# Kernel tuning notes

Measured on AMD Instinct MI355X. Metric: run time of the kernel, lower is better.

Reference implementation:

```python
import jax, jax.numpy as jnp
import numpy as np

EMBED = 1024
HEADS = 16
HEAD_DIM = EMBED // HEADS
N, SEQ = 4, 2048


def setup_inputs() -> dict:
    key = jax.random.key(0)
    ks = jax.random.split(key, 9)
    values = jax.random.normal(ks[0], (N, SEQ, EMBED), dtype=jnp.float32)
    keys = jax.random.normal(ks[1], (N, SEQ, EMBED), dtype=jnp.float32)
    query = jax.random.normal(ks[2], (N, SEQ, EMBED), dtype=jnp.float32)
    mask = jax.random.randint(ks[3], (N, 1, SEQ, SEQ), 0, 2, dtype=jnp.int32)
    s_h = 1.0 / np.sqrt(HEAD_DIM)
    s_e = 1.0 / np.sqrt(EMBED)
    Wv = jax.random.normal(ks[4], (HEAD_DIM, HEAD_DIM), dtype=jnp.float32) * s_h
    Wk = jax.random.normal(ks[5], (HEAD_DIM, HEAD_DIM), dtype=jnp.float32) * s_h
    Wq = jax.random.normal(ks[6], (HEAD_DIM, HEAD_DIM), dtype=jnp.float32) * s_h
    Wo = jax.random.normal(ks[7], (EMBED, EMBED), dtype=jnp.float32) * s_e
    bo = jax.random.normal(ks[8], (EMBED,), dtype=jnp.float32) * 0.01
    return {"values": values, "keys": keys, "query": query, "mask": mask,
            "Wv": Wv, "Wk": Wk, "Wq": Wq, "Wo": Wo, "bo": bo}


def reference(values, keys, query, mask, Wv, Wk, Wq, Wo, bo):
    n, q_len = query.shape[0], query.shape[1]
    k_len, v_len = keys.shape[1], values.shape[1]
    # split heads: [N, L, H, D]
    v = values.reshape(n, v_len, HEADS, HEAD_DIM)
    k = keys.reshape(n, k_len, HEADS, HEAD_DIM)
    q = query.reshape(n, q_len, HEADS, HEAD_DIM)
    # per-head linear projections (nn.Linear: x @ W.T)
    v = jnp.einsum('nlhd,ed->nlhe', v, Wv)
    k = jnp.einsum('nlhd,ed->nlhe', k, Wk)
    q = jnp.einsum('nlhd,ed->nlhe', q, Wq)
    # [N, H, Q, K] scores
    energy = jnp.einsum('nqhd,nkhd->nhqk', q, k)
    energy = jnp.where(mask == 0, jnp.float32(-1e20), energy)
    # note: original scales by sqrt(embed_size), not sqrt(head_dim)
    attention = jax.nn.softmax(energy / jnp.sqrt(jnp.float32(EMBED)), axis=3)
    out = jnp.einsum('nhql,nlhd->nqhd', attention, v).reshape(n, q_len, EMBED)
    return out @ Wo.T + bo
```

## Files before the change

### kernel.cpp

```cpp
#include <hip/hip_runtime.h>
#include <hip/hip_bf16.h>

typedef __attribute__((ext_vector_type(8))) short bfx8;
typedef __attribute__((ext_vector_type(4))) float fx4;

#define MFMA16(a,b,c) __builtin_amdgcn_mfma_f32_16x16x32_bf16((a),(b),(c),0,0,0)

__device__ __forceinline__ unsigned short bfc(float x){
  return __builtin_bit_cast(unsigned short, __float2bfloat16(x));
}
__device__ __forceinline__ unsigned pack2(float a, float b){
  return (unsigned)bfc(a) | ((unsigned)bfc(b) << 16);
}

__device__ __forceinline__ bfx8 cvt8(const float* p){
  const float4* q = (const float4*)p;
  float4 a = q[0], b = q[1];
  bfx8 r;
  r[0]=(short)bfc(a.x); r[1]=(short)bfc(a.y); r[2]=(short)bfc(a.z); r[3]=(short)bfc(a.w);
  r[4]=(short)bfc(b.x); r[5]=(short)bfc(b.y); r[6]=(short)bfc(b.z); r[7]=(short)bfc(b.w);
  return r;
}

__device__ __forceinline__ void g2l16(const void* g, void* l){
  __builtin_amdgcn_global_load_lds((const __attribute__((address_space(1))) unsigned*)g,
                                   (__attribute__((address_space(3))) unsigned*)l, 16, 0, 0);
}

#define SCL 0.04508422002778f

__global__ __launch_bounds__(256) void pack_k(const int* __restrict__ M, const float* __restrict__ Wo,
                                              unsigned long long* __restrict__ mT,
                                              unsigned short* __restrict__ Wob){
  int bid = blockIdx.x, tid = threadIdx.x;
  if (bid < 1024){
    int l = tid & 63, wv = tid >> 6;
    int task = bid*4 + wv;
    int n = task >> 10, rem = task & 1023, kt = rem >> 5, qc = rem & 31;
    int qbase = qc*64;
    const int* mp = M + (size_t)n*2048*2048 + (size_t)kt*64 + l;
    unsigned long long myw = 0;
    for (int qq = 0; qq < 64; ++qq){
      unsigned long long b = __ballot(mp[(size_t)(qbase+qq)*2048] != 0);
      if (l == qq) myw = b;
    }
    mT[((size_t)n*32 + kt)*2048 + qbase + l] = myw;
  } else {
    int i = ((bid-1024)*256 + tid)*8;
    bfx8 v = cvt8(Wo + i);
    *(bfx8*)(Wob + i) = v;
  }
}

__global__ __launch_bounds__(256) void proj_k(const float* __restrict__ Xv, const float* __restrict__ Xk,
                                              const float* __restrict__ Xq,
                                              const float* __restrict__ Wv, const float* __restrict__ Wk,
                                              const float* __restrict__ Wq,
                                              unsigned short* __restrict__ Vt, unsigned short* __restrict__ Kb,
                                              unsigned short* __restrict__ Qb){
  int bid = blockIdx.x;
  int which = bid >> 10;
  int r = bid & 1023;
  int nh = r >> 4, sb = r & 15;
  int n = nh >> 4, h = nh & 15;
  int tid = threadIdx.x, l = tid & 63, wv = tid >> 6, g = l >> 4, j = l & 15;
  const float* X = (which==0) ? Xv : ((which==1) ? Xk : Xq);
  const float* W = (which==0) ? Wv : ((which==1) ? Wk : Wq);
  int s0 = sb*128 + wv*32;
  size_t xbase = (size_t)n*2048*1024 + (size_t)h*64;

  if (which){
    float sc = (which==2) ? SCL : 1.0f;
    bfx8 bw[4][2];
    for (int nt=0;nt<4;++nt) for (int ks=0;ks<2;++ks)
      bw[nt][ks] = cvt8(W + (nt*16 + j)*64 + ks*32 + g*8);
    bfx8 ax[2][2];
    for (int mt=0;mt<2;++mt){
      const float* xp = X + xbase + (size_t)(s0 + mt*16 + j)*1024;
      for (int ks=0;ks<2;++ks) ax[mt][ks] = cvt8(xp + ks*32 + g*8);
    }
    fx4 acc[2][4];
    for (int mt=0;mt<2;++mt) for (int nt=0;nt<4;++nt) acc[mt][nt] = (fx4){0.f,0.f,0.f,0.f};
    for (int mt=0;mt<2;++mt) for (int nt=0;nt<4;++nt) for (int ks=0;ks<2;++ks)
      acc[mt][nt] = MFMA16(ax[mt][ks], bw[nt][ks], acc[mt][nt]);
    unsigned short* O = ((which==1) ? Kb : Qb) + (size_t)nh*2048*64;
    for (int mt=0;mt<2;++mt) for (int nt=0;nt<4;++nt) for (int rr=0;rr<4;++rr){
      int s = s0 + mt*16 + g*4 + rr, e = nt*16 + j;
      O[(size_t)s*64 + e] = bfc(acc[mt][nt][rr]*sc);
    }
  } else {
    bfx8 aw[4][2];
    for (int mt=0;mt<4;++mt) for (int ks=0;ks<2;++ks)
      aw[mt][ks] = cvt8(W + (mt*16 + j)*64 + ks*32 + g*8);
    bfx8 bx[2][2];
    for (int nt=0;nt<2;++nt){
      const float* xp = X + xbase + (size_t)(s0 + nt*16 + j)*1024;
      for (int ks=0;ks<2;++ks) bx[nt][ks] = cvt8(xp + ks*32 + g*8);
    }
    fx4 acc[4][2];
    for (int mt=0;mt<4;++mt) for (int nt=0;nt<2;++nt) acc[mt][nt] = (fx4){0.f,0.f,0.f,0.f};
    for (int mt=0;mt<4;++mt) for (int nt=0;nt<2;++nt) for (int ks=0;ks<2;++ks)
      acc[mt][nt] = MFMA16(aw[mt][ks], bx[nt][ks], acc[mt][nt]);
    unsigned short* O = Vt + (size_t)nh*64*2048;
    for (int mt=0;mt<4;++mt) for (int nt=0;nt<2;++nt) for (int rr=0;rr<4;++rr){
      int d = mt*16 + g*4 + rr, s = s0 + nt*16 + j;
      O[(size_t)d*2048 + s] = bfc(acc[mt][nt][rr]);
    }
  }
}

__global__ __launch_bounds__(512, 4) void flash_k(const unsigned short* __restrict__ Qb,
                                                  const unsigned short* __restrict__ Kb,
                                                  const unsigned short* __restrict__ Vt,
                                                  const unsigned long long* __restrict__ mT,
                                                  unsigned short* __restrict__ AO){
  __shared__ short lK[2][64*64];
  __shared__ short lV[2][64*64];
  __shared__ unsigned lP[8][1024];
  int tid = threadIdx.x;
  int l = tid & 63, wv = tid >> 6, g = l >> 4, j = l & 15;
  int bid = blockIdx.x;
  int nh = bid >> 3, qb = bid & 7;
  int n = nh >> 4, h = nh & 15;
  const unsigned short* Qp = Qb + (size_t)nh*2048*64;
  const unsigned short* Kp = Kb + (size_t)nh*2048*64;
  const unsigned short* Vp = Vt + (size_t)nh*64*2048;
  int q0 = qb*256 + wv*32 + j;
  bfx8 qf0[2], qf1[2];
  qf0[0] = *(const bfx8*)(Qp + (size_t)q0*64 + g*8);
  qf0[1] = *(const bfx8*)(Qp + (size_t)q0*64 + 32 + g*8);
  qf1[0] = *(const bfx8*)(Qp + (size_t)(q0+16)*64 + g*8);
  qf1[1] = *(const bfx8*)(Qp + (size_t)(q0+16)*64 + 32 + g*8);
  bfx8 ones;
  #pragma unroll
  for (int i=0;i<8;++i) ones[i] = (short)0x3F80;
  fx4 accO0[4], accO1[4];
  #pragma unroll
  for (int mt=0;mt<4;++mt){ accO0[mt] = (fx4){0.f,0.f,0.f,0.f}; accO1[mt] = (fx4){0.f,0.f,0.f,0.f}; }
  fx4 acc5a = (fx4){0.f,0.f,0.f,0.f};
  fx4 acc5b = (fx4){0.f,0.f,0.f,0.f};
  const int swz = (j & 7) << 4;
  const unsigned long long* mrow0 = mT + (size_t)n*32*2048 + q0;

  int sidx = wv*64 + l;
  int srow = sidx >> 3, scs = (sidx & 7) ^ (srow & 7);
  const unsigned short* Ksrc = Kp + (size_t)srow*64 + scs*8;
  const unsigned short* Vsrc = Vp + (size_t)srow*2048 + scs*8;

  #define STAGE(b, kt) do { \
    g2l16(Ksrc + (size_t)(kt)*4096, (char*)lK[b] + sidx*16); \
    g2l16(Vsrc + (size_t)(kt)*64,   (char*)lV[b] + sidx*16); \
  } while(0)

  STAGE(0, 0);
  __syncthreads();
  int b = 0;

  for (int kt = 0; kt < 32; ++kt){
    if (kt < 31) STAGE(b^1, kt+1);
    unsigned long long mw0 = mrow0[(size_t)kt*2048];
    unsigned long long mw1 = mrow0[(size_t)kt*2048 + 16];
    fx4 st0[4], st1[4];
    #pragma unroll
    for (int mt=0;mt<4;++mt){
      fx4 z0 = (fx4){0.f,0.f,0.f,0.f}, z1 = (fx4){0.f,0.f,0.f,0.f};
      #pragma unroll
      for (int ks=0;ks<2;++ks){
        bfx8 kf = *(const bfx8*)((const char*)lK[b] + (mt*16+j)*128 + ((ks*64 + g*16) ^ swz));
        z0 = MFMA16(kf, qf0[ks], z0);
        z1 = MFMA16(kf, qf1[ks], z1);
      }
      st0[mt] = z0; st1[mt] = z1;
    }
    unsigned* Pb = lP[wv];
    #pragma unroll
    for (int mt=0;mt<4;++mt){
      unsigned mq = (unsigned)(mw0 >> (mt*16 + g*4)) & 0xFu;
      float p0 = __builtin_amdgcn_exp2f(((mq>>0)&1u) ? st0[mt][0] : -1e30f);
      float p1 = __builtin_amdgcn_exp2f(((mq>>1)&1u) ? st0[mt][1] : -1e30f);
      float p2 = __builtin_amdgcn_exp2f(((mq>>2)&1u) ? st0[mt][2] : -1e30f);
      float p3 = __builtin_amdgcn_exp2f(((mq>>3)&1u) ? st0[mt][3] : -1e30f);
      int b0 = mt*32 + g*8;
      int addr = j*128 + ((((b0 >> 4)) ^ (j & 7)) << 4) + (b0 & 15);
      uint2 w; w.x = pack2(p0, p1); w.y = pack2(p2, p3);
      *(uint2*)((char*)Pb + addr) = w;
    }
    #pragma unroll
    for (int mt=0;mt<4;++mt){
      unsigned mq = (unsigned)(mw1 >> (mt*16 + g*4)) & 0xFu;
      float p0 = __builtin_amdgcn_exp2f(((mq>>0)&1u) ? st1[mt][0] : -1e30f);
      float p1 = __builtin_amdgcn_exp2f(((mq>>1)&1u) ? st1[mt][1] : -1e30f);
      float p2 = __builtin_amdgcn_exp2f(((mq>>2)&1u) ? st1[mt][2] : -1e30f);
      float p3 = __builtin_amdgcn_exp2f(((mq>>3)&1u) ? st1[mt][3] : -1e30f);
      int b0 = mt*32 + g*8;
      int addr = 2048 + j*128 + ((((b0 >> 4)) ^ (j & 7)) << 4) + (b0 & 15);
      uint2 w; w.x = pack2(p0, p1); w.y = pack2(p2, p3);
      *(uint2*)((char*)Pb + addr) = w;
    }
    bfx8 pf0[2], pf1[2];
    #pragma unroll
    for (int k2=0;k2<2;++k2){
      int boff = k2*64 + g*16;
      int addr = j*128 + ((((boff>>4)) ^ (j&7)) << 4);
      pf0[k2] = *(const bfx8*)((const char*)Pb + addr);
      pf1[k2] = *(const bfx8*)((const char*)Pb + 2048 + addr);
    }
    #pragma unroll
    for (int mt=0;mt<4;++mt)
      #pragma unroll
      for (int k2=0;k2<2;++k2){
        bfx8 vf = *(const bfx8*)((const char*)lV[b] + (mt*16+j)*128 + ((k2*64 + g*16) ^ swz));
        accO0[mt] = MFMA16(vf, pf0[k2], accO0[mt]);
        accO1[mt] = MFMA16(vf, pf1[k2], accO1[mt]);
      }
    acc5a = MFMA16(ones, pf0[0], acc5a);
    acc5a = MFMA16(ones, pf0[1], acc5a);
    acc5b = MFMA16(ones, pf1[0], acc5b);
    acc5b = MFMA16(ones, pf1[1], acc5b);
    __syncthreads();
    b ^= 1;
  }
  #undef STAGE

  float inv0 = 1.0f / acc5a[0];
  float inv1 = 1.0f / acc5b[0];
  size_t tok0 = (size_t)n*2048 + (size_t)qb*256 + wv*32 + j;
  #pragma unroll
  for (int mt=0;mt<4;++mt){
    ushort4 o;
    o.x = bfc(accO0[mt][0]*inv0); o.y = bfc(accO0[mt][1]*inv0);
    o.z = bfc(accO0[mt][2]*inv0); o.w = bfc(accO0[mt][3]*inv0);
    *(ushort4*)(AO + tok0*1024 + h*64 + mt*16 + g*4) = o;
    ushort4 o1;
    o1.x = bfc(accO1[mt][0]*inv1); o1.y = bfc(accO1[mt][1]*inv1);
    o1.z = bfc(accO1[mt][2]*inv1); o1.w = bfc(accO1[mt][3]*inv1);
    *(ushort4*)(AO + (tok0+16)*1024 + h*64 + mt*16 + g*4) = o1;
  }
}

__global__ __launch_bounds__(256) void gemm_k(const unsigned short* __restrict__ AO,
                                              const unsigned short* __restrict__ Wob,
                                              const float* __restrict__ bo, float* __restrict__ out){
  __shared__ short lA[2][128*32], lB[2][128*32];
  int tid = threadIdx.x, l = tid & 63, wv = tid >> 6, g = l >> 4, j = l & 15;
  int wr = wv >> 1, wc = wv & 1;
  int bid = blockIdx.x;
  int m0 = (bid >> 3)*128, n0 = (bid & 7)*128;
  fx4 acc[4][4];
  #pragma unroll
  for (int mt=0;mt<4;++mt) for (int nt=0;nt<4;++nt) acc[mt][nt] = (fx4){0.f,0.f,0.f,0.f};

  int sbase = wv*128;
  int sidx0 = sbase + l, sidx1 = sbase + 64 + l;
  int srow0 = sidx0 >> 2, sc0 = sidx0 & 3;
  int srow1 = sidx1 >> 2, sc1 = sidx1 & 3;
  const unsigned short* Asrc0 = AO  + (size_t)(m0+srow0)*1024 + sc0*8;
  const unsigned short* Asrc1 = AO  + (size_t)(m0+srow1)*1024 + sc1*8;
  const unsigned short* Bsrc0 = Wob + (size_t)(n0+srow0)*1024 + sc0*8;
  const unsigned short* Bsrc1 = Wob + (size_t)(n0+srow1)*1024 + sc1*8;

  #define GSTAGE(b, kb) do { \
    g2l16(Asrc0 + (kb)*32, (char*)lA[b] + sidx0*16); \
    g2l16(Asrc1 + (kb)*32, (char*)lA[b] + sidx1*16); \
    g2l16(Bsrc0 + (kb)*32, (char*)lB[b] + sidx0*16); \
    g2l16(Bsrc1 + (kb)*32, (char*)lB[b] + sidx1*16); \
  } while(0)

  GSTAGE(0, 0);
  __syncthreads();
  int b = 0;
  for (int kb = 0; kb < 32; ++kb){
    if (kb < 31) GSTAGE(b^1, kb+1);
    bfx8 af[4], bfr[4];
    #pragma unroll
    for (int mt=0;mt<4;++mt) af[mt]  = *(const bfx8*)((const char*)lA[b] + (wr*64 + mt*16 + j)*64 + g*16);
    #pragma unroll
    for (int nt=0;nt<4;++nt) bfr[nt] = *(const bfx8*)((const char*)lB[b] + (wc*64 + nt*16 + j)*64 + g*16);
    #pragma unroll
    for (int mt=0;mt<4;++mt)
      #pragma unroll
      for (int nt=0;nt<4;++nt)
        acc[mt][nt] = MFMA16(af[mt], bfr[nt], acc[mt][nt]);
    __syncthreads();
    b ^= 1;
  }
  #undef GSTAGE

  #pragma unroll
  for (int mt=0;mt<4;++mt)
    #pragma unroll
    for (int nt=0;nt<4;++nt){
      int mm = m0 + wr*64 + mt*16 + g*4;
      int oo = n0 + wc*64 + nt*16 + j;
      float bb = bo[oo];
      #pragma unroll
      for (int rr=0;rr<4;++rr)
        out[(size_t)(mm+rr)*1024 + oo] = acc[mt][nt][rr] + bb;
    }
}

extern "C" void kernel_launch(void* const* d_in, const int* in_sizes, int n_in,
                              void* d_out, int out_size, void* d_ws, size_t ws_size,
                              hipStream_t stream){
  const float* V  = (const float*)d_in[0];
  const float* K  = (const float*)d_in[1];
  const float* Q  = (const float*)d_in[2];
  const int*   M  = (const int*)d_in[3];
  const float* Wv = (const float*)d_in[4];
  const float* Wk = (const float*)d_in[5];
  const float* Wq = (const float*)d_in[6];
  const float* Wo = (const float*)d_in[7];
  const float* bo = (const float*)d_in[8];

  char* ws = (char*)d_ws;
  unsigned short* Qb = (unsigned short*)(ws + ((size_t)0  << 20));
  unsigned short* Kb = (unsigned short*)(ws + ((size_t)16 << 20));
  unsigned short* Vt = (unsigned short*)(ws + ((size_t)32 << 20));
  unsigned short* AO = (unsigned short*)(ws + ((size_t)48 << 20));
  unsigned long long* mT = (unsigned long long*)(ws + ((size_t)64 << 20));
  unsigned short* Wob = (unsigned short*)(ws + ((size_t)66 << 20));

  hipLaunchKernelGGL(pack_k,  dim3(1536), dim3(256), 0, stream, M, Wo, mT, Wob);
  hipLaunchKernelGGL(proj_k,  dim3(3072), dim3(256), 0, stream, V, K, Q, Wv, Wk, Wq, Vt, Kb, Qb);
  hipLaunchKernelGGL(flash_k, dim3(512),  dim3(512), 0, stream, Qb, Kb, Vt, mT, AO);
  hipLaunchKernelGGL(gemm_k,  dim3(512),  dim3(256), 0, stream, AO, Wob, bo, (float*)d_out);
}
```

Baseline: 202.0 us.

## Switch flash attention to 32x32 MFMA with register P-shuffle and merge prep kernels

Rewrites the attention kernel around 32x32x16 bf16 MFMA tiles. The probability tile now goes from the score accumulator to the PV operand through a lane xor-32 shuffle in registers, which removes the per-wave LDS staging buffer. The row sum is now accumulated in scalar registers instead of through extra MFMAs with a ones vector, and the mask is applied by bitmasking the exp result. The mask-pack and projection kernels are also fused into one launch to save a kernel boundary. The risks are higher register pressure from the 16-wide accumulators and the cost of the shuffles.

```diff
diff --git a/kernel.cpp b/kernel.cpp
--- a/kernel.cpp
+++ b/kernel.cpp
@@ -3,8 +3,11 @@
 
 typedef __attribute__((ext_vector_type(8))) short bfx8;
 typedef __attribute__((ext_vector_type(4))) float fx4;
+typedef __attribute__((ext_vector_type(16))) float f32x16;
+typedef __attribute__((ext_vector_type(4))) unsigned u32x4;
 
 #define MFMA16(a,b,c) __builtin_amdgcn_mfma_f32_16x16x32_bf16((a),(b),(c),0,0,0)
+#define MFMA32(a,b,c) __builtin_amdgcn_mfma_f32_32x32x16_bf16((a),(b),(c),0,0,0)
 
 __device__ __forceinline__ unsigned short bfc(float x){
   return __builtin_bit_cast(unsigned short, __float2bfloat16(x));
@@ -12,7 +15,6 @@
 __device__ __forceinline__ unsigned pack2(float a, float b){
   return (unsigned)bfc(a) | ((unsigned)bfc(b) << 16);
 }
-
 __device__ __forceinline__ bfx8 cvt8(const float* p){
   const float4* q = (const float4*)p;
   float4 a = q[0], b = q[1];
@@ -21,49 +23,59 @@
   r[4]=(short)bfc(b.x); r[5]=(short)bfc(b.y); r[6]=(short)bfc(b.z); r[7]=(short)bfc(b.w);
   return r;
 }
-
 __device__ __forceinline__ void g2l16(const void* g, void* l){
   __builtin_amdgcn_global_load_lds((const __attribute__((address_space(1))) unsigned*)g,
                                    (__attribute__((address_space(3))) unsigned*)l, 16, 0, 0);
 }
+__device__ __forceinline__ float mexp(float zv, unsigned mws, int pos){
+  float e = __builtin_amdgcn_exp2f(zv);
+  unsigned msk = (unsigned)(((int)(mws << (31-pos))) >> 31);
+  return __builtin_bit_cast(float, __builtin_bit_cast(unsigned, e) & msk);
+}
+__device__ __forceinline__ f32x16 zero16(){
+  f32x16 z;
+  #pragma unroll
+  for (int i=0;i<16;++i) z[i] = 0.f;
+  return z;
+}
 
 #define SCL 0.04508422002778f
 
-__global__ __launch_bounds__(256) void pack_k(const int* __restrict__ M, const float* __restrict__ Wo,
-                                              unsigned long long* __restrict__ mT,
-                                              unsigned short* __restrict__ Wob){
-  int bid = blockIdx.x, tid = threadIdx.x;
-  if (bid < 1024){
-    int l = tid & 63, wv = tid >> 6;
-    int task = bid*4 + wv;
-    int n = task >> 10, rem = task & 1023, kt = rem >> 5, qc = rem & 31;
-    int qbase = qc*64;
-    const int* mp = M + (size_t)n*2048*2048 + (size_t)kt*64 + l;
-    unsigned long long myw = 0;
-    for (int qq = 0; qq < 64; ++qq){
-      unsigned long long b = __ballot(mp[(size_t)(qbase+qq)*2048] != 0);
-      if (l == qq) myw = b;
-    }
-    mT[((size_t)n*32 + kt)*2048 + qbase + l] = myw;
-  } else {
-    int i = ((bid-1024)*256 + tid)*8;
-    bfx8 v = cvt8(Wo + i);
-    *(bfx8*)(Wob + i) = v;
-  }
-}
-
-__global__ __launch_bounds__(256) void proj_k(const float* __restrict__ Xv, const float* __restrict__ Xk,
+__global__ __launch_bounds__(256) void prep_k(const float* __restrict__ Xv, const float* __restrict__ Xk,
                                               const float* __restrict__ Xq,
                                               const float* __restrict__ Wv, const float* __restrict__ Wk,
                                               const float* __restrict__ Wq,
+                                              const int* __restrict__ M, const float* __restrict__ Wo,
                                               unsigned short* __restrict__ Vt, unsigned short* __restrict__ Kb,
-                                              unsigned short* __restrict__ Qb){
+                                              unsigned short* __restrict__ Qb,
+                                              unsigned long long* __restrict__ mT,
+                                              unsigned short* __restrict__ Wob){
   int bid = blockIdx.x;
+  int tid = threadIdx.x, l = tid & 63, wv = tid >> 6, g = l >> 4, j = l & 15;
+  if (bid >= 3072){
+    int pid = bid - 3072;
+    if (pid < 1024){
+      int task = pid*4 + wv;
+      int n = task >> 10, rem = task & 1023, kt = rem >> 5, qc = rem & 31;
+      int qbase = qc*64;
+      const int* mp = M + (size_t)n*2048*2048 + (size_t)kt*64 + l;
+      unsigned long long myw = 0;
+      for (int qq = 0; qq < 64; ++qq){
+        unsigned long long b = __ballot(mp[(size_t)(qbase+qq)*2048] != 0);
+        if (l == qq) myw = b;
+      }
+      mT[((size_t)n*32 + kt)*2048 + qbase + l] = myw;
+    } else {
+      int i = ((pid-1024)*256 + tid)*8;
+      bfx8 v = cvt8(Wo + i);
+      *(bfx8*)(Wob + i) = v;
+    }
+    return;
+  }
   int which = bid >> 10;
   int r = bid & 1023;
   int nh = r >> 4, sb = r & 15;
   int n = nh >> 4, h = nh & 15;
-  int tid = threadIdx.x, l = tid & 63, wv = tid >> 6, g = l >> 4, j = l & 15;
   const float* X = (which==0) ? Xv : ((which==1) ? Xk : Xq);
   const float* W = (which==0) ? Wv : ((which==1) ? Wk : Wq);
   int s0 = sb*128 + wv*32;
@@ -116,125 +128,110 @@
                                                   unsigned short* __restrict__ AO){
   __shared__ short lK[2][64*64];
   __shared__ short lV[2][64*64];
-  __shared__ unsigned lP[8][1024];
   int tid = threadIdx.x;
-  int l = tid & 63, wv = tid >> 6, g = l >> 4, j = l & 15;
+  int l = tid & 63, wv = tid >> 6, hi = l >> 5, c = l & 31;
+  int cl7 = c & 7, hi4 = hi*4;
   int bid = blockIdx.x;
   int nh = bid >> 3, qb = bid & 7;
   int n = nh >> 4, h = nh & 15;
-  const unsigned short* Qp = Qb + (size_t)nh*2048*64;
-  const unsigned short* Kp = Kb + (size_t)nh*2048*64;
-  const unsigned short* Vp = Vt + (size_t)nh*64*2048;
-  int q0 = qb*256 + wv*32 + j;
-  bfx8 qf0[2], qf1[2];
-  qf0[0] = *(const bfx8*)(Qp + (size_t)q0*64 + g*8);
-  qf0[1] = *(const bfx8*)(Qp + (size_t)q0*64 + 32 + g*8);
-  qf1[0] = *(const bfx8*)(Qp + (size_t)(q0+16)*64 + g*8);
-  qf1[1] = *(const bfx8*)(Qp + (size_t)(q0+16)*64 + 32 + g*8);
-  bfx8 ones;
-  #pragma unroll
-  for (int i=0;i<8;++i) ones[i] = (short)0x3F80;
-  fx4 accO0[4], accO1[4];
-  #pragma unroll
-  for (int mt=0;mt<4;++mt){ accO0[mt] = (fx4){0.f,0.f,0.f,0.f}; accO1[mt] = (fx4){0.f,0.f,0.f,0.f}; }
-  fx4 acc5a = (fx4){0.f,0.f,0.f,0.f};
-  fx4 acc5b = (fx4){0.f,0.f,0.f,0.f};
-  const int swz = (j & 7) << 4;
-  const unsigned long long* mrow0 = mT + (size_t)n*32*2048 + q0;
+  const unsigned short* Qp = Qb + (size_t)nh*131072;
+  const unsigned short* Kp = Kb + (size_t)nh*131072;
+  const unsigned short* Vp = Vt + (size_t)nh*131072;
+  int q = qb*256 + wv*32 + c;
+  bfx8 qf[4];
+  #pragma unroll
+  for (int s=0;s<4;++s) qf[s] = *(const bfx8*)(Qp + (size_t)q*64 + s*16 + hi*8);
+  f32x16 accO0 = zero16(), accO1 = zero16();
+  float ls = 0.f;
+  const unsigned long long* mrow = mT + (size_t)n*65536 + q;
+  int rowK0 = c*128;
+  int rowK1 = rowK0 + 4096;
 
   int sidx = wv*64 + l;
   int srow = sidx >> 3, scs = (sidx & 7) ^ (srow & 7);
   const unsigned short* Ksrc = Kp + (size_t)srow*64 + scs*8;
   const unsigned short* Vsrc = Vp + (size_t)srow*2048 + scs*8;
 
-  #define STAGE(b, kt) do { \
-    g2l16(Ksrc + (size_t)(kt)*4096, (char*)lK[b] + sidx*16); \
-    g2l16(Vsrc + (size_t)(kt)*64,   (char*)lV[b] + sidx*16); \
+  g2l16(Ksrc, (char*)lK[0] + sidx*16);
+  g2l16(Vsrc, (char*)lV[0] + sidx*16);
+  __syncthreads();
+
+#define PROC_TILE(zz, mws, TT, VB) do { \
+    unsigned Wt[8]; \
+    _Pragma("unroll") \
+    for (int wi=0; wi<8; ++wi){ \
+      const int r0 = 2*wi; \
+      const int pos = (r0&3) + 8*(r0>>2); \
+      float p0_ = mexp((zz)[r0],   (mws), pos); \
+      float p1_ = mexp((zz)[r0+1], (mws), pos+1); \
+      ls += p0_ + p1_; \
+      Wt[wi] = pack2(p0_, p1_); \
+    } \
+    _Pragma("unroll") \
+    for (int mm=0; mm<2; ++mm){ \
+      unsigned xa = hi ? Wt[4*mm+0] : Wt[4*mm+2]; \
+      unsigned xb = hi ? Wt[4*mm+1] : Wt[4*mm+3]; \
+      unsigned ra = (unsigned)__shfl_xor((int)xa, 32); \
+      unsigned rb = (unsigned)__shfl_xor((int)xb, 32); \
+      u32x4 pw; \
+      pw.x = hi ? ra : Wt[4*mm+0]; \
+      pw.y = hi ? rb : Wt[4*mm+1]; \
+      pw.z = hi ? Wt[4*mm+2] : ra; \
+      pw.w = hi ? Wt[4*mm+3] : rb; \
+      bfx8 pb = __builtin_bit_cast(bfx8, pw); \
+      const int ch2 = 2*((TT)*2+mm); \
+      bfx8 vf0 = *(const bfx8*)((VB) + rowK0 + (((ch2+hi) ^ cl7) << 4)); \
+      bfx8 vf1 = *(const bfx8*)((VB) + rowK1 + (((ch2+hi) ^ cl7) << 4)); \
+      accO0 = MFMA32(vf0, pb, accO0); \
+      accO1 = MFMA32(vf1, pb, accO1); \
+    } \
   } while(0)
 
-  STAGE(0, 0);
-  __syncthreads();
-  int b = 0;
-
-  for (int kt = 0; kt < 32; ++kt){
-    if (kt < 31) STAGE(b^1, kt+1);
-    unsigned long long mw0 = mrow0[(size_t)kt*2048];
-    unsigned long long mw1 = mrow0[(size_t)kt*2048 + 16];
-    fx4 st0[4], st1[4];
-    #pragma unroll
-    for (int mt=0;mt<4;++mt){
-      fx4 z0 = (fx4){0.f,0.f,0.f,0.f}, z1 = (fx4){0.f,0.f,0.f,0.f};
-      #pragma unroll
-      for (int ks=0;ks<2;++ks){
-        bfx8 kf = *(const bfx8*)((const char*)lK[b] + (mt*16+j)*128 + ((ks*64 + g*16) ^ swz));
-        z0 = MFMA16(kf, qf0[ks], z0);
-        z1 = MFMA16(kf, qf1[ks], z1);
-      }
-      st0[mt] = z0; st1[mt] = z1;
-    }
-    unsigned* Pb = lP[wv];
-    #pragma unroll
-    for (int mt=0;mt<4;++mt){
-      unsigned mq = (unsigned)(mw0 >> (mt*16 + g*4)) & 0xFu;
-      float p0 = __builtin_amdgcn_exp2f(((mq>>0)&1u) ? st0[mt][0] : -1e30f);
-      float p1 = __builtin_amdgcn_exp2f(((mq>>1)&1u) ? st0[mt][1] : -1e30f);
-      float p2 = __builtin_amdgcn_exp2f(((mq>>2)&1u) ? st0[mt][2] : -1e30f);
-      float p3 = __builtin_amdgcn_exp2f(((mq>>3)&1u) ? st0[mt][3] : -1e30f);
-      int b0 = mt*32 + g*8;
-      int addr = j*128 + ((((b0 >> 4)) ^ (j & 7)) << 4) + (b0 & 15);
-      uint2 w; w.x = pack2(p0, p1); w.y = pack2(p2, p3);
-      *(uint2*)((char*)Pb + addr) = w;
-    }
-    #pragma unroll
-    for (int mt=0;mt<4;++mt){
-      unsigned mq = (unsigned)(mw1 >> (mt*16 + g*4)) & 0xFu;
-      float p0 = __builtin_amdgcn_exp2f(((mq>>0)&1u) ? st1[mt][0] : -1e30f);
-      float p1 = __builtin_amdgcn_exp2f(((mq>>1)&1u) ? st1[mt][1] : -1e30f);
-      float p2 = __builtin_amdgcn_exp2f(((mq>>2)&1u) ? st1[mt][2] : -1e30f);
-      float p3 = __builtin_amdgcn_exp2f(((mq>>3)&1u) ? st1[mt][3] : -1e30f);
-      int b0 = mt*32 + g*8;
-      int addr = 2048 + j*128 + ((((b0 >> 4)) ^ (j & 7)) << 4) + (b0 & 15);
-      uint2 w; w.x = pack2(p0, p1); w.y = pack2(p2, p3);
-      *(uint2*)((char*)Pb + addr) = w;
-    }
-    bfx8 pf0[2], pf1[2];
-    #pragma unroll
-    for (int k2=0;k2<2;++k2){
-      int boff = k2*64 + g*16;
-      int addr = j*128 + ((((boff>>4)) ^ (j&7)) << 4);
-      pf0[k2] = *(const bfx8*)((const char*)Pb + addr);
-      pf1[k2] = *(const bfx8*)((const char*)Pb + 2048 + addr);
-    }
-    #pragma unroll
-    for (int mt=0;mt<4;++mt)
-      #pragma unroll
-      for (int k2=0;k2<2;++k2){
-        bfx8 vf = *(const bfx8*)((const char*)lV[b] + (mt*16+j)*128 + ((k2*64 + g*16) ^ swz));
-        accO0[mt] = MFMA16(vf, pf0[k2], accO0[mt]);
-        accO1[mt] = MFMA16(vf, pf1[k2], accO1[mt]);
-      }
-    acc5a = MFMA16(ones, pf0[0], acc5a);
-    acc5a = MFMA16(ones, pf0[1], acc5a);
-    acc5b = MFMA16(ones, pf1[0], acc5b);
-    acc5b = MFMA16(ones, pf1[1], acc5b);
-    __syncthreads();
-    b ^= 1;
-  }
-  #undef STAGE
-
-  float inv0 = 1.0f / acc5a[0];
-  float inv1 = 1.0f / acc5b[0];
-  size_t tok0 = (size_t)n*2048 + (size_t)qb*256 + wv*32 + j;
-  #pragma unroll
-  for (int mt=0;mt<4;++mt){
+#define ATTN_ITER(BUF, NBUF, kt) do { \
+    if ((kt) < 31){ \
+      g2l16(Ksrc + (size_t)((kt)+1)*4096, (char*)lK[NBUF] + sidx*16); \
+      g2l16(Vsrc + (size_t)((kt)+1)*64,   (char*)lV[NBUF] + sidx*16); \
+    } \
+    unsigned long long mw = mrow[(size_t)(kt)*2048]; \
+    const char* KB = (const char*)lK[BUF]; \
+    const char* VB = (const char*)lV[BUF]; \
+    f32x16 z0 = zero16(), z1 = zero16(); \
+    _Pragma("unroll") \
+    for (int s=0; s<4; ++s){ \
+      bfx8 kf0 = *(const bfx8*)(KB + rowK0 + (((2*s+hi) ^ cl7) << 4)); \
+      bfx8 kf1 = *(const bfx8*)(KB + rowK1 + (((2*s+hi) ^ cl7) << 4)); \
+      z0 = MFMA32(kf0, qf[s], z0); \
+      z1 = MFMA32(kf1, qf[s], z1); \
+    } \
+    unsigned mws0 = ((unsigned)mw) >> hi4; \
+    unsigned mws1 = ((unsigned)(mw >> 32)) >> hi4; \
+    PROC_TILE(z0, mws0, 0, VB); \
+    PROC_TILE(z1, mws1, 1, VB); \
+    __syncthreads(); \
+  } while(0)
+
+  #pragma unroll 1
+  for (int kt2 = 0; kt2 < 32; kt2 += 2){
+    ATTN_ITER(0, 1, kt2);
+    ATTN_ITER(1, 0, kt2+1);
+  }
+#undef ATTN_ITER
+#undef PROC_TILE
+
+  ls += __shfl_xor(ls, 32);
+  float inv = 1.0f / ls;
+  unsigned short* aop = AO + ((size_t)n*2048 + q)*1024 + h*64;
+  #pragma unroll
+  for (int u=0; u<4; ++u){
+    int d0 = u*8 + hi4;
     ushort4 o;
-    o.x = bfc(accO0[mt][0]*inv0); o.y = bfc(accO0[mt][1]*inv0);
-    o.z = bfc(accO0[mt][2]*inv0); o.w = bfc(accO0[mt][3]*inv0);
-    *(ushort4*)(AO + tok0*1024 + h*64 + mt*16 + g*4) = o;
+    o.x = bfc(accO0[4*u+0]*inv); o.y = bfc(accO0[4*u+1]*inv);
+    o.z = bfc(accO0[4*u+2]*inv); o.w = bfc(accO0[4*u+3]*inv);
+    *(ushort4*)(aop + d0) = o;
     ushort4 o1;
-    o1.x = bfc(accO1[mt][0]*inv1); o1.y = bfc(accO1[mt][1]*inv1);
-    o1.z = bfc(accO1[mt][2]*inv1); o1.w = bfc(accO1[mt][3]*inv1);
-    *(ushort4*)(AO + (tok0+16)*1024 + h*64 + mt*16 + g*4) = o1;
+    o1.x = bfc(accO1[4*u+0]*inv); o1.y = bfc(accO1[4*u+1]*inv);
+    o1.z = bfc(accO1[4*u+2]*inv); o1.w = bfc(accO1[4*u+3]*inv);
+    *(ushort4*)(aop + 32 + d0) = o1;
   }
 }
 
@@ -320,8 +317,8 @@
   unsigned long long* mT = (unsigned long long*)(ws + ((size_t)64 << 20));
   unsigned short* Wob = (unsigned short*)(ws + ((size_t)66 << 20));
 
-  hipLaunchKernelGGL(pack_k,  dim3(1536), dim3(256), 0, stream, M, Wo, mT, Wob);
-  hipLaunchKernelGGL(proj_k,  dim3(3072), dim3(256), 0, stream, V, K, Q, Wv, Wk, Wq, Vt, Kb, Qb);
+  hipLaunchKernelGGL(prep_k,  dim3(4608), dim3(256), 0, stream,
+                     V, K, Q, Wv, Wk, Wq, M, Wo, Vt, Kb, Qb, mT, Wob);
   hipLaunchKernelGGL(flash_k, dim3(512),  dim3(512), 0, stream, Qb, Kb, Vt, mT, AO);
   hipLaunchKernelGGL(gemm_k,  dim3(512),  dim3(256), 0, stream, AO, Wob, bo, (float*)d_out);
 }
```

Result: faster. 192.8 us (-4.5%).
